# Kernel optimization log

Hardware: AMD Instinct MI355X
Metric: run time of the kernel (lower is better)

Reference implementation:

```python
import jax, jax.numpy as jnp
import numpy as np

B, N, D_IN, D_MID, D_OUT = 512, 8192, 128, 256, 16


def setup_inputs() -> dict:
    key = jax.random.key(0)
    k1, k2, k3, k4, k5 = jax.random.split(key, 5)
    return {
        "x": jax.random.normal(k1, (B, D_IN), dtype=jnp.float32),
        "calc_X": jax.random.normal(k2, (N, D_IN), dtype=jnp.float32),
        "calc_Y": jax.random.normal(k3, (N, D_OUT), dtype=jnp.float32),
        "W1": jax.random.normal(k4, (D_MID, D_IN), dtype=jnp.float32) * (D_IN ** -0.5),
        "W2": jax.random.normal(k5, (D_OUT, D_MID), dtype=jnp.float32) * (D_MID ** -0.5),
        "h": jnp.array([1.5], dtype=jnp.float32),
    }


def _mlp(v, W1, W2):
    # fc2(relu(fc1(v))), both linears bias-free
    return jnp.maximum(v @ W1.T, 0.0) @ W2.T


def reference(x, calc_X, calc_Y, W1, W2, h):
    Zw = _mlp(x, W1, W2)        # [B, D_OUT] queries
    Xw = _mlp(calc_X, W1, W2)   # [N, D_OUT] reference embeddings (batched, no loop)
    # Gaussian kernel weights gauss((Xw_j - Zw)/h): [B, N, D_OUT]
    z = (Xw[None, :, :] - Zw[:, None, :]) / h
    w = jnp.exp(-0.5 * z * z)
    denominator = jnp.sum(w, axis=1)                   # [B, D_OUT]
    numerator = jnp.einsum("bnd,nd->bd", w, calc_Y)    # [B, D_OUT]
    return numerator / denominator
```

## Files before the change

kernel.cpp:

```cpp
#include <hip/hip_runtime.h>

#define D_IN  128
#define D_MID 256
#define D_OUT 16
#define NB    512
#define NN    8192
#define NROWS (NB + NN)
#define RPB   16
#define BT    8
#define NSLICE 8
#define SLICE_N (NN / NSLICE)

#define EW_OFF    0
#define PART_OFF  (NROWS * D_OUT)
#define W1T_OFF   (PART_OFF + 2 * NSLICE * NB * D_OUT)
#define W2T_OFF   (W1T_OFF + D_MID * D_IN)

__global__ __launch_bounds__(256) void transpose_kernel(
    const float* __restrict__ W1, const float* __restrict__ W2,
    float* __restrict__ W1T, float* __restrict__ W2T)
{
    const int tid = blockIdx.x * 256 + threadIdx.x;
    if (tid < 8192) {
        const int k4 = tid >> 8;
        const int j  = tid & 255;
        const float4 v = reinterpret_cast<const float4*>(W1)[(size_t)j * 32 + k4];
        reinterpret_cast<float4*>(W1T)[(size_t)k4 * 256 + j] = v;
    } else {
        const int t2 = tid - 8192;
        const int j4 = t2 >> 4;
        const int d  = t2 & 15;
        const float4 v = reinterpret_cast<const float4*>(W2)[(size_t)d * 64 + j4];
        reinterpret_cast<float4*>(W2T)[(size_t)j4 * 16 + d] = v;
    }
}

__global__ __launch_bounds__(256) void mlp_kernel(
    const float* __restrict__ x, const float* __restrict__ calc_X,
    const float* __restrict__ W1T, const float* __restrict__ W2T,
    const float* __restrict__ hptr, float* __restrict__ Ews)
{
    __shared__ float hid[RPB][260];

    const int t = threadIdx.x;
    const int row0 = blockIdx.x * RPB;

    const float* __restrict__ rbase = (row0 < NB)
        ? (x + (size_t)row0 * D_IN)
        : (calc_X + (size_t)(row0 - NB) * D_IN);
    const float4* __restrict__ row4 = reinterpret_cast<const float4*>(rbase);
    const float4* __restrict__ w1t4 = reinterpret_cast<const float4*>(W1T);

    float acc[RPB] = {};
#pragma unroll 2
    for (int k4 = 0; k4 < 32; ++k4) {
        const float4 wv = w1t4[k4 * 256 + t];
#pragma unroll
        for (int r = 0; r < RPB; ++r) {
            const float4 rv = row4[r * 32 + k4];
            acc[r] = fmaf(rv.x, wv.x, fmaf(rv.y, wv.y,
                     fmaf(rv.z, wv.z, fmaf(rv.w, wv.w, acc[r]))));
        }
    }
#pragma unroll
    for (int r = 0; r < RPB; ++r)
        hid[r][t] = fmaxf(acc[r], 0.f);
    __syncthreads();

    {
        const int r = t >> 4;
        const int d = t & 15;
        const float4* __restrict__ w2t4 = reinterpret_cast<const float4*>(W2T);
        float4 a = make_float4(0.f, 0.f, 0.f, 0.f);
#pragma unroll 8
        for (int j4 = 0; j4 < 64; ++j4) {
            const float4 wv = w2t4[j4 * 16 + d];
            const float4 hv = *reinterpret_cast<const float4*>(&hid[r][j4 * 4]);
            a.x = fmaf(hv.x, wv.x, a.x);
            a.y = fmaf(hv.y, wv.y, a.y);
            a.z = fmaf(hv.z, wv.z, a.z);
            a.w = fmaf(hv.w, wv.w, a.w);
        }
        const float s = 0.84932180028801904272f / hptr[0];
        Ews[(size_t)(row0 + r) * D_OUT + d] = ((a.x + a.y) + (a.z + a.w)) * s;
    }
}

__global__ __launch_bounds__(256) void kde_kernel(
    const float* __restrict__ Ews, const float* __restrict__ Y,
    float* __restrict__ partial)
{
    __shared__ float red[4][16][16];

    const int t     = threadIdx.x;
    const int d     = t & 15;
    const int chunk = t >> 4;
    const int b0    = blockIdx.x * BT;
    const int slice = blockIdx.y;
    const float* __restrict__ Xws = Ews + (size_t)NB * D_OUT;

    float z[BT], num[BT] = {}, den[BT] = {};
#pragma unroll
    for (int bt = 0; bt < BT; ++bt)
        z[bt] = Ews[(size_t)(b0 + bt) * D_OUT + d];

#pragma unroll 4
    for (int i = 0; i < SLICE_N / 16; ++i) {
        const int n = slice * SLICE_N + i * 16 + chunk;
        const float xw = Xws[(size_t)n * D_OUT + d];
        const float yv = Y[(size_t)n * D_OUT + d];
#pragma unroll
        for (int bt = 0; bt < BT; ++bt) {
            const float df = xw - z[bt];
            const float w  = __builtin_amdgcn_exp2f(-(df * df));
            den[bt] += w;
            num[bt] = fmaf(w, yv, num[bt]);
        }
    }

    float vals[16];
#pragma unroll
    for (int bt = 0; bt < BT; ++bt) {
        vals[bt * 2 + 0] = num[bt];
        vals[bt * 2 + 1] = den[bt];
    }
#pragma unroll
    for (int m = 16; m <= 32; m <<= 1) {
#pragma unroll
        for (int v = 0; v < 16; ++v)
            vals[v] += __shfl_xor(vals[v], m, 64);
    }

    const int wave = t >> 6;
    if ((t & 63) < 16) {
#pragma unroll
        for (int v = 0; v < 16; ++v) red[wave][d][v] = vals[v];
    }
    __syncthreads();

    {
        const int p  = t & 1;
        const int dd = (t >> 1) & 15;
        const int bt = t >> 5;
        const int v  = bt * 2 + p;
        const float sum = red[0][dd][v] + red[1][dd][v] + red[2][dd][v] + red[3][dd][v];
        partial[(size_t)(p * NSLICE + slice) * NB * D_OUT + (size_t)(b0 + bt) * D_OUT + dd] = sum;
    }
}

__global__ __launch_bounds__(256) void combine_kernel(
    const float* __restrict__ partial, float* __restrict__ out)
{
    const int i = blockIdx.x * 256 + threadIdx.x;
    float nsum = 0.f, dsum = 0.f;
#pragma unroll
    for (int s = 0; s < NSLICE; ++s) {
        nsum += partial[(size_t)s * NB * D_OUT + i];
        dsum += partial[(size_t)(NSLICE + s) * NB * D_OUT + i];
    }
    out[i] = nsum / dsum;
}

extern "C" void kernel_launch(void* const* d_in, const int* in_sizes, int n_in,
                              void* d_out, int out_size, void* d_ws, size_t ws_size,
                              hipStream_t stream) {
    const float* x      = (const float*)d_in[0];
    const float* calc_X = (const float*)d_in[1];
    const float* calc_Y = (const float*)d_in[2];
    const float* W1     = (const float*)d_in[3];
    const float* W2     = (const float*)d_in[4];
    const float* h      = (const float*)d_in[5];

    float* ws      = (float*)d_ws;
    float* Ews     = ws + EW_OFF;
    float* partial = ws + PART_OFF;
    float* W1T     = ws + W1T_OFF;
    float* W2T     = ws + W2T_OFF;
    float* out     = (float*)d_out;

    transpose_kernel<<<dim3(36), dim3(256), 0, stream>>>(W1, W2, W1T, W2T);
    mlp_kernel<<<dim3(NROWS / RPB), dim3(256), 0, stream>>>(x, calc_X, W1T, W2T, h, Ews);
    kde_kernel<<<dim3(NB / BT, NSLICE), dim3(256), 0, stream>>>(Ews, calc_Y, partial);
    combine_kernel<<<dim3(NB * D_OUT / 256), dim3(256), 0, stream>>>(partial, out);
}
```

Baseline: 54.71 us.

## Split MLP into LDS-tiled register-blocked fc1 GEMM and separate fc2 kernel

```diff
diff --git a/kernel.cpp b/kernel.cpp
--- a/kernel.cpp
+++ b/kernel.cpp
@@ -6,13 +6,13 @@
 #define NB    512
 #define NN    8192
 #define NROWS (NB + NN)
-#define RPB   16
 #define BT    8
 #define NSLICE 8
 #define SLICE_N (NN / NSLICE)
 
-#define EW_OFF    0
-#define PART_OFF  (NROWS * D_OUT)
+#define HID_OFF   0
+#define EW_OFF    (NROWS * D_MID)
+#define PART_OFF  (EW_OFF + NROWS * D_OUT)
 #define W1T_OFF   (PART_OFF + 2 * NSLICE * NB * D_OUT)
 #define W2T_OFF   (W1T_OFF + D_MID * D_IN)
 
@@ -25,7 +25,10 @@
         const int k4 = tid >> 8;
         const int j  = tid & 255;
         const float4 v = reinterpret_cast<const float4*>(W1)[(size_t)j * 32 + k4];
-        reinterpret_cast<float4*>(W1T)[(size_t)k4 * 256 + j] = v;
+        W1T[(size_t)(k4 * 4 + 0) * D_MID + j] = v.x;
+        W1T[(size_t)(k4 * 4 + 1) * D_MID + j] = v.y;
+        W1T[(size_t)(k4 * 4 + 2) * D_MID + j] = v.z;
+        W1T[(size_t)(k4 * 4 + 3) * D_MID + j] = v.w;
     } else {
         const int t2 = tid - 8192;
         const int j4 = t2 >> 4;
@@ -35,54 +38,147 @@
     }
 }
 
-__global__ __launch_bounds__(256) void mlp_kernel(
+__global__ __launch_bounds__(256) void fc1_kernel(
     const float* __restrict__ x, const float* __restrict__ calc_X,
-    const float* __restrict__ W1T, const float* __restrict__ W2T,
-    const float* __restrict__ hptr, float* __restrict__ Ews)
-{
-    __shared__ float hid[RPB][260];
-
-    const int t = threadIdx.x;
-    const int row0 = blockIdx.x * RPB;
+    const float* __restrict__ W1T, float* __restrict__ hidden)
+{
+    __shared__ float rows[32][132];
+    __shared__ float w1lds[2][32][128];
+
+    const int t    = threadIdx.x;
+    const int rb   = blockIdx.x >> 1;
+    const int ch   = blockIdx.x & 1;
+    const int row0 = rb * 32;
+    const int wave = t >> 6;
+    const int lane = t & 63;
+    const int tg_r = t >> 5;
+    const int tg_c = t & 31;
 
     const float* __restrict__ rbase = (row0 < NB)
         ? (x + (size_t)row0 * D_IN)
         : (calc_X + (size_t)(row0 - NB) * D_IN);
-    const float4* __restrict__ row4 = reinterpret_cast<const float4*>(rbase);
-    const float4* __restrict__ w1t4 = reinterpret_cast<const float4*>(W1T);
-
-    float acc[RPB] = {};
-#pragma unroll 2
-    for (int k4 = 0; k4 < 32; ++k4) {
-        const float4 wv = w1t4[k4 * 256 + t];
-#pragma unroll
-        for (int r = 0; r < RPB; ++r) {
-            const float4 rv = row4[r * 32 + k4];
-            acc[r] = fmaf(rv.x, wv.x, fmaf(rv.y, wv.y,
-                     fmaf(rv.z, wv.z, fmaf(rv.w, wv.w, acc[r]))));
-        }
-    }
-#pragma unroll
-    for (int r = 0; r < RPB; ++r)
-        hid[r][t] = fmaxf(acc[r], 0.f);
+
+    {
+        const float4* __restrict__ row4 = reinterpret_cast<const float4*>(rbase);
+#pragma unroll
+        for (int q = 0; q < 4; ++q) {
+            const int idx = t + q * 256;
+            const float4 v = row4[idx];
+            *reinterpret_cast<float4*>(&rows[idx >> 5][(idx & 31) * 4]) = v;
+        }
+    }
+
+    const float4* __restrict__ w1g = reinterpret_cast<const float4*>(W1T + ch * 128);
+
+    float4 wreg[4];
+#define LOAD_PANEL(p)                                                   \
+    {                                                                   \
+        _Pragma("unroll")                                               \
+        for (int q = 0; q < 4; ++q) {                                   \
+            const int idx = (wave * 4 + q) * 64 + lane;                 \
+            const int kk  = idx >> 5;                                   \
+            const int c4  = idx & 31;                                   \
+            wreg[q] = w1g[(size_t)((p) * 32 + kk) * 64 + c4];           \
+        }                                                               \
+    }
+#define WRITE_PANEL(buf)                                                \
+    {                                                                   \
+        _Pragma("unroll")                                               \
+        for (int q = 0; q < 4; ++q) {                                   \
+            const int idx = (wave * 4 + q) * 64 + lane;                 \
+            const int kk  = idx >> 5;                                   \
+            const int c4  = idx & 31;                                   \
+            *reinterpret_cast<float4*>(&w1lds[buf][kk][c4 * 4]) = wreg[q]; \
+        }                                                               \
+    }
+
+    LOAD_PANEL(0);
+    WRITE_PANEL(0);
     __syncthreads();
 
-    {
-        const int r = t >> 4;
-        const int d = t & 15;
-        const float4* __restrict__ w2t4 = reinterpret_cast<const float4*>(W2T);
-        float4 a = make_float4(0.f, 0.f, 0.f, 0.f);
+    float acc[4][4] = {};
+    const int r0 = tg_r * 4;
+    const int c0 = tg_c * 4;
+
+    for (int p = 0; p < 4; ++p) {
+        const int buf = p & 1;
+        if (p < 3) LOAD_PANEL(p + 1);
 #pragma unroll 8
-        for (int j4 = 0; j4 < 64; ++j4) {
-            const float4 wv = w2t4[j4 * 16 + d];
-            const float4 hv = *reinterpret_cast<const float4*>(&hid[r][j4 * 4]);
-            a.x = fmaf(hv.x, wv.x, a.x);
-            a.y = fmaf(hv.y, wv.y, a.y);
-            a.z = fmaf(hv.z, wv.z, a.z);
-            a.w = fmaf(hv.w, wv.w, a.w);
-        }
+        for (int kk = 0; kk < 32; ++kk) {
+            const float4 wv = *reinterpret_cast<const float4*>(&w1lds[buf][kk][c0]);
+            const int k = p * 32 + kk;
+            const float r0v = rows[r0 + 0][k];
+            const float r1v = rows[r0 + 1][k];
+            const float r2v = rows[r0 + 2][k];
+            const float r3v = rows[r0 + 3][k];
+            acc[0][0] = fmaf(r0v, wv.x, acc[0][0]);
+            acc[0][1] = fmaf(r0v, wv.y, acc[0][1]);
+            acc[0][2] = fmaf(r0v, wv.z, acc[0][2]);
+            acc[0][3] = fmaf(r0v, wv.w, acc[0][3]);
+            acc[1][0] = fmaf(r1v, wv.x, acc[1][0]);
+            acc[1][1] = fmaf(r1v, wv.y, acc[1][1]);
+            acc[1][2] = fmaf(r1v, wv.z, acc[1][2]);
+            acc[1][3] = fmaf(r1v, wv.w, acc[1][3]);
+            acc[2][0] = fmaf(r2v, wv.x, acc[2][0]);
+            acc[2][1] = fmaf(r2v, wv.y, acc[2][1]);
+            acc[2][2] = fmaf(r2v, wv.z, acc[2][2]);
+            acc[2][3] = fmaf(r2v, wv.w, acc[2][3]);
+            acc[3][0] = fmaf(r3v, wv.x, acc[3][0]);
+            acc[3][1] = fmaf(r3v, wv.y, acc[3][1]);
+            acc[3][2] = fmaf(r3v, wv.z, acc[3][2]);
+            acc[3][3] = fmaf(r3v, wv.w, acc[3][3]);
+        }
+        __syncthreads();
+        if (p < 3) {
+            WRITE_PANEL(buf ^ 1);
+            __syncthreads();
+        }
+    }
+
+#pragma unroll
+    for (int i = 0; i < 4; ++i) {
+        float4 o;
+        o.x = fmaxf(acc[i][0], 0.f);
+        o.y = fmaxf(acc[i][1], 0.f);
+        o.z = fmaxf(acc[i][2], 0.f);
+        o.w = fmaxf(acc[i][3], 0.f);
+        *reinterpret_cast<float4*>(
+            hidden + (size_t)(row0 + r0 + i) * D_MID + ch * 128 + c0) = o;
+    }
+#undef LOAD_PANEL
+#undef WRITE_PANEL
+}
+
+__global__ __launch_bounds__(256) void fc2_kernel(
+    const float* __restrict__ hidden, const float* __restrict__ W2T,
+    const float* __restrict__ hptr, float* __restrict__ Ews)
+{
+    const int t    = threadIdx.x;
+    const int rloc = t >> 5;
+    const int half = (t >> 4) & 1;
+    const int d    = t & 15;
+    const int r    = blockIdx.x * 8 + rloc;
+
+    const float4* __restrict__ h4 =
+        reinterpret_cast<const float4*>(hidden + (size_t)r * D_MID) + half * 32;
+    const float4* __restrict__ w4 =
+        reinterpret_cast<const float4*>(W2T) + half * 32 * 16;
+
+    float4 a = make_float4(0.f, 0.f, 0.f, 0.f);
+#pragma unroll 8
+    for (int j4 = 0; j4 < 32; ++j4) {
+        const float4 hv = h4[j4];
+        const float4 wv = w4[j4 * 16 + d];
+        a.x = fmaf(hv.x, wv.x, a.x);
+        a.y = fmaf(hv.y, wv.y, a.y);
+        a.z = fmaf(hv.z, wv.z, a.z);
+        a.w = fmaf(hv.w, wv.w, a.w);
+    }
+    float v = (a.x + a.y) + (a.z + a.w);
+    v += __shfl_xor(v, 16, 64);
+    if (half == 0) {
         const float s = 0.84932180028801904272f / hptr[0];
-        Ews[(size_t)(row0 + r) * D_OUT + d] = ((a.x + a.y) + (a.z + a.w)) * s;
+        Ews[(size_t)r * D_OUT + d] = v * s;
     }
 }
 
@@ -172,6 +268,7 @@
     const float* h      = (const float*)d_in[5];
 
     float* ws      = (float*)d_ws;
+    float* hidden  = ws + HID_OFF;
     float* Ews     = ws + EW_OFF;
     float* partial = ws + PART_OFF;
     float* W1T     = ws + W1T_OFF;
@@ -179,7 +276,8 @@
     float* out     = (float*)d_out;
 
     transpose_kernel<<<dim3(36), dim3(256), 0, stream>>>(W1, W2, W1T, W2T);
-    mlp_kernel<<<dim3(NROWS / RPB), dim3(256), 0, stream>>>(x, calc_X, W1T, W2T, h, Ews);
+    fc1_kernel<<<dim3(544), dim3(256), 0, stream>>>(x, calc_X, W1T, hidden);
+    fc2_kernel<<<dim3(NROWS / 8), dim3(256), 0, stream>>>(hidden, W2T, h, Ews);
     kde_kernel<<<dim3(NB / BT, NSLICE), dim3(256), 0, stream>>>(Ews, calc_Y, partial);
     combine_kernel<<<dim3(NB * D_OUT / 256), dim3(256), 0, stream>>>(partial, out);
 }
```

After: 59.37 us. +8.5%, slower.
